# Kernel optimization log

Hardware: AMD Instinct MI355X
Metric: run time of the kernel (lower is better)

Reference implementation:

```python
import jax, jax.numpy as jnp
import numpy as np
from jax import lax

EPS = 1e-5      # BatchNorm1d default eps
SLOPE = 0.01    # LeakyReLU default negative_slope
DN = ('NCDHW', 'OIDHW', 'NCDHW')
PAD_31 = ((1, 1), (0, 0), (1, 1))   # kernel (3,1,3), padding (1,0,1)
PAD_13 = ((0, 0), (1, 1), (1, 1))   # kernel (1,3,3), padding (0,1,1)
PAD_P = ((1, 1), (1, 1), (1, 1))    # pool kernel 3, padding 1
STRIDE_P = (2, 2, 1)                # height_pooling=False -> stride (2,2,1)


def setup_inputs() -> dict:
    key = jax.random.key(0)
    ks = jax.random.split(key, 8)
    B, Cin, Cout = 1, 32, 64
    D1, D2, D3 = 160, 160, 32
    mask = jax.random.randint(ks[0], (B, 1, D1, D2, D3), 0, 2) > 0
    x = jax.random.normal(ks[1], (B, Cin, D1, D2, D3), dtype=jnp.float32)

    def w(k, cin, cout, kd, kh, kw):
        return jax.random.normal(k, (cout, cin, kd, kh, kw), dtype=jnp.float32) * 0.05

    inp = {
        'x': x, 'mask': mask,
        'W_A1': w(ks[2], Cin, Cout, 3, 1, 3),
        'W_A2': w(ks[3], Cout, Cout, 1, 3, 3),
        'W_B1': w(ks[4], Cin, Cout, 1, 3, 3),
        'W_B2': w(ks[5], Cout, Cout, 3, 1, 3),
        'W_pool': w(ks[6], Cout, Cout, 3, 3, 3),
    }
    for name in ('A1', 'A2', 'B1', 'B2'):
        inp['g_' + name] = jnp.ones((Cout,), jnp.float32)
        inp['b_' + name] = jnp.zeros((Cout,), jnp.float32)
    return inp


def _conv(h, W, pad, stride=(1, 1, 1)):
    return lax.conv_general_dilated(h, W, stride, pad, dimension_numbers=DN)


def _lrelu(h):
    return jnp.where(h >= 0, h, SLOPE * h)


def _masked_bn(h, m, n_active, gamma, beta):
    # BatchNorm1d over the [N_active, C] sparse feature tensor:
    # per-channel stats over active voxels only (biased variance, training mode).
    mean = jnp.sum(h * m, axis=(0, 2, 3, 4)) / n_active
    mu = mean[None, :, None, None, None]
    var = jnp.sum(((h - mu) ** 2) * m, axis=(0, 2, 3, 4)) / n_active
    inv = lax.rsqrt(var + EPS)[None, :, None, None, None]
    out = (h - mu) * inv * gamma[None, :, None, None, None] + beta[None, :, None, None, None]
    return out * m  # keep inactive sites exactly zero


def reference(x, mask, W_A1, W_A2, W_B1, W_B2, W_pool,
              g_A1, b_A1, g_A2, b_A2, g_B1, b_B1, g_B2, b_B2):
    m = mask.astype(x.dtype)                      # [B,1,D1,D2,D3] active-site indicator
    n_active = jnp.sum(m)
    xs = x * m                                    # sparse input: zero at inactive voxels

    def subm(h, W, pad):
        # submanifold conv: compute only at active output sites (same site set as input)
        return _conv(h, W, pad) * m

    # branch A: conv3x1 -> LeakyReLU -> BN -> conv1x3 -> LeakyReLU -> BN
    res_A = _masked_bn(_lrelu(subm(xs, W_A1, PAD_31)), m, n_active, g_A1, b_A1)
    res_A = _masked_bn(_lrelu(subm(res_A, W_A2, PAD_13)), m, n_active, g_A2, b_A2)

    # branch B: conv1x3 -> LeakyReLU -> BN -> conv3x1 -> LeakyReLU -> BN
    res_B = _masked_bn(_lrelu(subm(xs, W_B1, PAD_13)), m, n_active, g_B1, b_B1)
    res_B = _masked_bn(_lrelu(subm(res_B, W_B2, PAD_31)), m, n_active, g_B2, b_B2)

    res_B = res_B + res_A

    # strided SparseConv3d pool: output active where any input in 3x3x3 window is active
    ones_k = jnp.ones((1, 1, 3, 3, 3), x.dtype)
    out_mask = (_conv(m, ones_k, PAD_P, STRIDE_P) > 0).astype(x.dtype)
    down = _conv(res_B, W_pool, PAD_P, STRIDE_P) * out_mask
    return (down, res_B)
```

## Files before the change

kernel.cpp:

```cpp
#include <hip/hip_runtime.h>

static constexpr int ND1=160, ND2=160, ND3=32;
static constexpr int SP  = ND1*ND2*ND3;
static constexpr int CO  = 64;
static constexpr int OD1=80, OD2=80, OD3=32;
static constexpr int OSP = OD1*OD2*OD3;
static constexpr int NSC = 64;

typedef __attribute__((ext_vector_type(8))) short  short8;
typedef __attribute__((ext_vector_type(4))) float  f32x4;

__device__ __forceinline__ float b2f_lo(unsigned u){ return __uint_as_float(u<<16); }
__device__ __forceinline__ float b2f_hi(unsigned u){ return __uint_as_float(u & 0xffff0000u); }
__device__ __forceinline__ unsigned short f2b(float f){
    unsigned u = __float_as_uint(f);
    u += 0x7fffu + ((u>>16)&1u);
    return (unsigned short)(u>>16);
}
__device__ __forceinline__ unsigned cvtpk(float lo, float hi){
    unsigned r;
    asm("v_cvt_pk_bf16_f32 %0, %1, %2" : "=v"(r) : "v"(lo), "v"(hi));
    return r;
}
__device__ __forceinline__ float lrelu(float x){ return fmaxf(x, 0.01f*x); }

__global__ void k_detect(const unsigned char* __restrict__ mb, int* __restrict__ flag)
{
    __shared__ int lf;
    if (threadIdx.x == 0) lf = 0;
    __syncthreads();
    int f = 0;
    for (int i = blockIdx.x*256 + threadIdx.x; i < SP; i += gridDim.x*256) {
        unsigned char b = mb[i];
        if (b > 1) f |= 4;
        if (b != 0 && (i & 3)) f |= 1;
    }
    if (f) atomicOr(&lf, f);
    __syncthreads();
    if (threadIdx.x == 0 && lf) atomicOr(flag, lf);
}

__global__ void k_mask(const void* __restrict__ mraw, const int* __restrict__ flag,
                       float* __restrict__ m, float* __restrict__ nactN)
{
    int i = blockIdx.x*256 + threadIdx.x;
    int f = *flag;
    float v;
    if (f & 4)      v = (reinterpret_cast<const float*>(mraw)[i] != 0.f) ? 1.f : 0.f;
    else if (f & 1) v = (reinterpret_cast<const unsigned char*>(mraw)[i] != 0) ? 1.f : 0.f;
    else            v = (reinterpret_cast<const int*>(mraw)[i] != 0) ? 1.f : 0.f;
    m[i] = v;
    float s = v;
    #pragma unroll
    for (int off = 32; off > 0; off >>= 1) s += __shfl_xor(s, off);
    __shared__ float wsum[4];
    if ((threadIdx.x & 63) == 0) wsum[threadIdx.x >> 6] = s;
    __syncthreads();
    if (threadIdx.x == 0) atomicAdd(&nactN[blockIdx.x & (NSC-1)], wsum[0]+wsum[1]+wsum[2]+wsum[3]);
}

__global__ void k_finalize2(const float* __restrict__ SN0, const float* __restrict__ g0,
                            const float* __restrict__ b0, float* __restrict__ o0,
                            const float* __restrict__ SN1, const float* __restrict__ g1,
                            const float* __restrict__ b1, float* __restrict__ o1,
                            const float* __restrict__ nactN)
{
    const float* SN = blockIdx.x ? SN1 : SN0;
    const float* g  = blockIdx.x ? g1  : g0;
    const float* b  = blockIdx.x ? b1  : b0;
    float*       o  = blockIdx.x ? o1  : o0;
    int c = threadIdx.x;
    float s1 = 0.f, s2 = 0.f;
    #pragma unroll 4
    for (int k = 0; k < NSC; k++){
        s1 += SN[k*128 + c];
        s2 += SN[k*128 + 64 + c];
    }
    float nn = nactN[c];
    #pragma unroll
    for (int off = 32; off > 0; off >>= 1) nn += __shfl_xor(nn, off);
    float mean = s1 / nn;
    float var  = s2 / nn - mean*mean;
    float inv  = rsqrtf(var + 1e-5f);
    float sc   = inv * g[c];
    o[c]      = sc;
    o[64 + c] = b[c] - mean*sc;
}

__global__ void k_wprep_all(const float* __restrict__ WA1, const float* __restrict__ WA2,
                            const float* __restrict__ WB1, const float* __restrict__ WB2,
                            const float* __restrict__ WP,
                            unsigned short* __restrict__ tA1, unsigned short* __restrict__ tA2,
                            unsigned short* __restrict__ tB1, unsigned short* __restrict__ tB2,
                            unsigned short* __restrict__ tP)
{
    int i = blockIdx.x*256 + threadIdx.x;
    const float* W; unsigned short* Wt; int CIN, NT, base;
    if      (i < 18432)  { W=WA1; Wt=tA1; CIN=32; NT=9;  base=0; }
    else if (i < 55296)  { W=WA2; Wt=tA2; CIN=64; NT=9;  base=18432; }
    else if (i < 73728)  { W=WB1; Wt=tB1; CIN=32; NT=9;  base=55296; }
    else if (i < 110592) { W=WB2; Wt=tB2; CIN=64; NT=9;  base=73728; }
    else if (i < 221184) { W=WP;  Wt=tP;  CIN=64; NT=27; base=110592; }
    else return;
    int j = i - base;
    int ksub = j & 31;
    int t = j >> 5;
    int co = t & 63;
    int kc = t >> 6;
    int nch = CIN >> 5;
    int tap = kc / nch;
    int ci  = (kc - tap*nch)*32 + ksub;
    Wt[j] = f2b(W[((size_t)co*CIN + ci)*NT + tap]);
}

__global__ void k_prep_x(const float* __restrict__ x, const float* __restrict__ m,
                         unsigned short* __restrict__ xt, float* __restrict__ om)
{
    __shared__ float t[64][33];
    int sp0 = blockIdx.x*64;
    int tid = threadIdx.x;
    int c = tid>>6, s = tid&63;
    float mm = m[sp0+s];
    #pragma unroll
    for (int r=0;r<8;r++){
        int ci = c + r*4;
        t[s][ci] = x[(size_t)ci*SP + sp0 + s]*mm;
    }
    __syncthreads();
    int sp = tid>>2, c0 = (tid&3)*8;
    uint4 pk;
    pk.x = cvtpk(t[sp][c0+0], t[sp][c0+1]);
    pk.y = cvtpk(t[sp][c0+2], t[sp][c0+3]);
    pk.z = cvtpk(t[sp][c0+4], t[sp][c0+5]);
    pk.w = cvtpk(t[sp][c0+6], t[sp][c0+7]);
    *reinterpret_cast<uint4*>(xt + (size_t)(sp0+sp)*32 + c0) = pk;

    if (blockIdx.x < OSP/256){
        int i = blockIdx.x*256 + tid;
        int o3 = i & 31; int tt = i >> 5; int o2 = tt % OD2; int o1 = tt / OD2;
        float ssum = 0.f;
        for (int kd = 0; kd < 3; kd++) { int d1 = 2*o1 - 1 + kd; if ((unsigned)d1 >= ND1) continue;
          for (int kh = 0; kh < 3; kh++) { int d2 = 2*o2 - 1 + kh; if ((unsigned)d2 >= ND2) continue;
            for (int kw = 0; kw < 3; kw++) { int d3 = o3 - 1 + kw; if ((unsigned)d3 >= ND3) continue;
              ssum += m[(d1*ND2 + d2)*ND3 + d3];
            } } }
        om[i] = (ssum > 0.f) ? 1.f : 0.f;
    }
}

__global__ void k_resB(const unsigned short* __restrict__ hA, const unsigned short* __restrict__ hB,
                       const float* __restrict__ sA, const float* __restrict__ sB,
                       const float* __restrict__ m,
                       unsigned short* __restrict__ rbt, float* __restrict__ resf)
{
    __shared__ float t[64][65];
    __shared__ float ss[256];
    int tid = threadIdx.x;
    if (tid < 128){ ss[tid] = sA[tid]; ss[128+tid] = sB[tid]; }
    __syncthreads();
    int sp0 = blockIdx.x*64;
    int sp = tid>>2, c0 = (tid&3)*16;
    float mm = m[sp0+sp];
    const size_t base = (size_t)(sp0+sp)*64 + c0;
    uint4 a0 = *reinterpret_cast<const uint4*>(hA + base);
    uint4 a1 = *reinterpret_cast<const uint4*>(hA + base + 8);
    uint4 b0 = *reinterpret_cast<const uint4*>(hB + base);
    uint4 b1 = *reinterpret_cast<const uint4*>(hB + base + 8);
    unsigned pa4[8] = {a0.x,a0.y,a0.z,a0.w,a1.x,a1.y,a1.z,a1.w};
    unsigned pb4[8] = {b0.x,b0.y,b0.z,b0.w,b1.x,b1.y,b1.z,b1.w};
    float vv[16];
    #pragma unroll
    for (int q=0;q<8;q++){
        int ci = c0+q*2;
        float va0 = b2f_lo(pa4[q]), va1 = b2f_hi(pa4[q]);
        float vb0 = b2f_lo(pb4[q]), vb1 = b2f_hi(pb4[q]);
        float v0 = (va0*ss[ci]   + ss[64+ci]   + vb0*ss[128+ci]   + ss[192+ci])*mm;
        float v1 = (va1*ss[ci+1] + ss[64+ci+1] + vb1*ss[128+ci+1] + ss[192+ci+1])*mm;
        t[sp][ci] = v0; t[sp][ci+1] = v1;
        vv[q*2] = v0; vv[q*2+1] = v1;
    }
    uint4 p0, p1;
    p0.x = cvtpk(vv[0],vv[1]);   p0.y = cvtpk(vv[2],vv[3]);
    p0.z = cvtpk(vv[4],vv[5]);   p0.w = cvtpk(vv[6],vv[7]);
    p1.x = cvtpk(vv[8],vv[9]);   p1.y = cvtpk(vv[10],vv[11]);
    p1.z = cvtpk(vv[12],vv[13]); p1.w = cvtpk(vv[14],vv[15]);
    *reinterpret_cast<uint4*>(rbt + base)     = p0;
    *reinterpret_cast<uint4*>(rbt + base + 8) = p1;
    __syncthreads();
    int ci = tid>>2, s0 = (tid&3)*16;
    #pragma unroll
    for (int kq=0;kq<4;kq++){
        float4 ov;
        ov.x = t[s0+4*kq+0][ci]; ov.y = t[s0+4*kq+1][ci];
        ov.z = t[s0+4*kq+2][ci]; ov.w = t[s0+4*kq+3][ci];
        *reinterpret_cast<float4*>(resf + (size_t)ci*SP + sp0 + s0 + 4*kq) = ov;
    }
}

template<int CIN, bool HASAFF, int KA, int KB>
__launch_bounds__(256, 2)
__global__ void mconv_dual(const unsigned short* __restrict__ inA, const unsigned short* __restrict__ WtA,
                           const float* __restrict__ scshA, unsigned short* __restrict__ outA,
                           float* __restrict__ statsA,
                           const unsigned short* __restrict__ inB, const unsigned short* __restrict__ WtB,
                           const float* __restrict__ scshB, unsigned short* __restrict__ outB2,
                           float* __restrict__ statsB,
                           const float* __restrict__ mstage, const float* __restrict__ mout)
{
    constexpr int NCH  = CIN/32;
    constexpr int NR   = 10;
    constexpr int ROWB = 34*CIN*2;
    constexpr int SWZ  = (CIN==64) ? 7 : 3;
    constexpr int OBST = 144;
    constexpr int LDSZ = (NR*ROWB > 256*OBST) ? NR*ROWB : 256*OBST;
    __shared__ __align__(16) char lds[LDSZ];
    __shared__ float sst[128];

    const int tid = threadIdx.x;
    const int w = tid>>6, l = tid&63, g = l>>4, lj = l&15;

    const int bid  = blockIdx.x;
    const int hb   = (bid >= 3200) ? 1 : 0;
    const int b2   = bid - hb*3200;
    const int gi   = (b2&7)*400 + (b2>>3);
    const int kind = hb ? KB : KA;
    const unsigned short* in  = hb ? inB   : inA;
    const unsigned short* Wt  = hb ? WtB   : WtA;
    const float*        scsh  = hb ? scshB : scshA;
    unsigned short*     outb  = hb ? outB2 : outA;
    float*             statsN = hb ? statsB : statsA;

    int z  = gi % 160;
    int r0 = (gi / 160)*8;

    if (tid < 128) sst[tid] = 0.f;

    const int sd3 = tid>>3;
    const int k0  = (tid&7)*(CIN/8);

    float sc[8], sh[8];
    if (HASAFF){
        #pragma unroll
        for (int j=0;j<8;j++){ sc[j]=scsh[k0+j]; sh[j]=scsh[64+k0+j]; }
    }

    for (int i = tid; i < NR*2*(CIN/8); i += 256){
        int per = CIN/8;
        int rr = i / (2*per);
        int rem = i - rr*2*per;
        int slot = (rem >= per) ? 33 : 0;
        int kc16 = (rem >= per) ? (rem - per) : rem;
        int dst = rr*ROWB + slot*CIN*2 + kc16*16;
        dst ^= ((slot&SWZ)<<4);
        *reinterpret_cast<uint4*>(lds + dst) = make_uint4(0,0,0,0);
    }

    if (CIN==64){
        uint4 v[NR]; float mmr[NR];
        #pragma unroll
        for (int rr=0; rr<NR; rr++){
            int rw = r0 - 1 + rr;
            v[rr] = make_uint4(0,0,0,0); mmr[rr] = 0.f;
            if ((unsigned)rw < 160u){
                int vox = (kind==0) ? ((rw*ND2 + z)*ND3 + sd3)
                                    : ((z*ND2 + rw)*ND3 + sd3);
                v[rr] = *reinterpret_cast<const uint4*>(in + (size_t)vox*CIN + k0);
                if (HASAFF) mmr[rr] = mstage[vox];
            }
        }
        #pragma unroll
        for (int rr=0; rr<NR; rr++){
            uint4 vv = v[rr];
            if (HASAFF){
                float mm = mmr[rr];
                float q0 = (b2f_lo(vv.x)*sc[0]+sh[0])*mm;
                float q1 = (b2f_hi(vv.x)*sc[1]+sh[1])*mm;
                float q2 = (b2f_lo(vv.y)*sc[2]+sh[2])*mm;
                float q3 = (b2f_hi(vv.y)*sc[3]+sh[3])*mm;
                float q4 = (b2f_lo(vv.z)*sc[4]+sh[4])*mm;
                float q5 = (b2f_hi(vv.z)*sc[5]+sh[5])*mm;
                float q6 = (b2f_lo(vv.w)*sc[6]+sh[6])*mm;
                float q7 = (b2f_hi(vv.w)*sc[7]+sh[7])*mm;
                vv.x = cvtpk(q0,q1); vv.y = cvtpk(q2,q3);
                vv.z = cvtpk(q4,q5); vv.w = cvtpk(q6,q7);
            }
            int dst = (rr*ROWB + (((sd3+1)*CIN + k0)*2)) ^ (((sd3+1)&SWZ)<<4);
            *reinterpret_cast<uint4*>(lds + dst) = vv;
        }
    } else {
        uint2 v[NR];
        #pragma unroll
        for (int rr=0; rr<NR; rr++){
            int rw = r0 - 1 + rr;
            v[rr] = make_uint2(0,0);
            if ((unsigned)rw < 160u){
                int vox = (kind==0) ? ((rw*ND2 + z)*ND3 + sd3)
                                    : ((z*ND2 + rw)*ND3 + sd3);
                v[rr] = *reinterpret_cast<const uint2*>(in + (size_t)vox*CIN + k0);
            }
        }
        #pragma unroll
        for (int rr=0; rr<NR; rr++){
            int dst = (rr*ROWB + (((sd3+1)*CIN + k0)*2)) ^ (((sd3+1)&SWZ)<<4);
            *reinterpret_cast<uint2*>(lds + dst) = v[rr];
        }
    }

    int tb[4];
    #pragma unroll
    for (int t=0;t<4;t++){
        int rowb = w*2 + (t>>1);
        int o3   = (t&1)*16 + lj;
        tb[t] = rowb*ROWB + ((o3*CIN + g*8)*2);
    }

    __syncthreads();

    f32x4 acc[4][4];
    #pragma unroll
    for (int c=0;c<4;c++)
        #pragma unroll
        for (int t=0;t<4;t++)
            #pragma unroll
            for (int q=0;q<4;q++) acc[c][t][q] = 0.f;

    const unsigned short* wb = Wt + lj*32 + g*8;

    #pragma unroll 1
    for (int ch=0; ch<NCH; ch++){
        short8 pa[9][4];
        #pragma unroll
        for (int tap=0; tap<9; tap++){
            const int kc = tap*NCH + ch;
            #pragma unroll
            for (int ct=0; ct<4; ct++)
                pa[tap][ct] = *reinterpret_cast<const short8*>(wb + (size_t)kc*2048 + ct*512);
        }
        int f[3];
        #pragma unroll
        for (int kw=0;kw<3;kw++){
            int x   = (lj+kw)&SWZ;
            int fld = (CIN==64) ? (g + 4*ch) : g;
            f[kw] = kw*CIN*2 + ((CIN==64) ? ch*64 : 0) + (((fld ^ x) - fld) << 4);
        }
        #pragma unroll
        for (int tap=0; tap<9; tap++){
            const int kd = tap/3, kw = tap - kd*3;
            #pragma unroll
            for (int t=0;t<4;t++){
                short8 bv = *reinterpret_cast<const short8*>(lds + kd*ROWB + tb[t] + f[kw]);
                #pragma unroll
                for (int ct=0; ct<4; ct++)
                    acc[ct][t] = __builtin_amdgcn_mfma_f32_16x16x32_bf16(pa[tap][ct], bv, acc[ct][t], 0,0,0);
            }
        }
    }

    __syncthreads();

    float mmv[4];
    #pragma unroll
    for (int t=0;t<4;t++){
        int rowb = w*2 + (t>>1);
        int o3   = (t&1)*16 + lj;
        int o2r  = r0 + rowb;
        int ovox = (kind==0) ? ((o2r*ND2 + z)*ND3 + o3)
                             : ((z*ND2 + o2r)*ND3 + o3);
        mmv[t] = mout[ovox];
    }
    #pragma unroll
    for (int ct=0;ct<4;ct++){
        float s1[4] = {0.f,0.f,0.f,0.f};
        float s2[4] = {0.f,0.f,0.f,0.f};
        #pragma unroll
        for (int t=0;t<4;t++){
            int rowb = w*2 + (t>>1);
            int o3   = (t&1)*16 + lj;
            int vloc = rowb*32 + o3;
            float v[4];
            #pragma unroll
            for (int r=0;r<4;r++){
                float xv = lrelu(acc[ct][t][r]*mmv[t]);
                v[r] = xv; s1[r] += xv; s2[r] += xv*xv;
            }
            *reinterpret_cast<uint2*>(lds + vloc*OBST + (ct*16 + g*4)*2) =
                make_uint2(cvtpk(v[0],v[1]), cvtpk(v[2],v[3]));
        }
        #pragma unroll
        for (int r=0;r<4;r++){
            float a = s1[r], b = s2[r];
            a += __shfl_xor(a,1); b += __shfl_xor(b,1);
            a += __shfl_xor(a,2); b += __shfl_xor(b,2);
            a += __shfl_xor(a,4); b += __shfl_xor(b,4);
            a += __shfl_xor(a,8); b += __shfl_xor(b,8);
            if (lj == 0){
                atomicAdd(&sst[ct*16 + g*4 + r], a);
                atomicAdd(&sst[64 + ct*16 + g*4 + r], b);
            }
        }
    }
    __syncthreads();
    #pragma unroll
    for (int i=0;i<8;i++){
        int idx = i*256 + tid;
        int vloc = idx >> 3;
        int q    = idx & 7;
        int row  = vloc >> 5;
        int o3g  = vloc & 31;
        int gvox = (kind==0) ? (((r0+row)*ND2 + z)*ND3 + o3g)
                             : ((z*ND2 + (r0+row))*ND3 + o3g);
        uint4 v = *reinterpret_cast<uint4*>(lds + vloc*OBST + q*16);
        *reinterpret_cast<uint4*>(outb + (size_t)gvox*64 + q*8) = v;
    }
    if (tid < 128){
        float* sg = statsN + (size_t)(blockIdx.x & (NSC-1))*128;
        atomicAdd(&sg[tid], sst[tid]);
    }
}

__launch_bounds__(256, 2)
__global__ void mpool5(const unsigned short* __restrict__ in,
                       const unsigned short* __restrict__ Wt,
                       const float* __restrict__ mout,
                       float* __restrict__ outf)
{
    constexpr int SLOTB = 80;
    constexpr int ROWB  = 34*SLOTB;
    extern __shared__ __align__(16) char lds[];

    const int tid = threadIdx.x;
    const int w = tid>>6, l = tid&63, g = l>>4, lj = l&15;
    const int h = w&1, rg = w>>1;

    int gi = (blockIdx.x & 7)*(gridDim.x>>3) + (blockIdx.x>>3);
    int z  = gi % OD1;
    int r0 = (gi / OD1)*4;

    const int sd3 = tid>>3;
    const int kq  = tid&7;

    for (int i = tid; i < 27*2*4; i += 256){
        int row = i >> 3, rem = i & 7;
        int slot = (rem >= 4) ? 33 : 0;
        int c16 = rem & 3;
        *reinterpret_cast<uint4*>(lds + row*ROWB + slot*SLOTB + c16*16) = make_uint4(0,0,0,0);
    }

    int ovx[4];
    float om[4];
    #pragma unroll
    for (int t=0;t<4;t++){
        int row = rg*2 + (t>>1);
        int o3  = (t&1)*16 + lj;
        ovx[t] = (z*OD2 + (r0 + row))*OD3 + o3;
        om[t]  = mout[ovx[t]];
    }

    f32x4 acc[2][4];
    #pragma unroll
    for (int c=0;c<2;c++)
        #pragma unroll
        for (int t=0;t<4;t++)
            #pragma unroll
            for (int q=0;q<4;q++) acc[c][t][q] = 0.f;

    const unsigned short* wbase = Wt + (size_t)(h*32)*32 + lj*32 + g*8;

    #pragma unroll 1
    for (int ph=0; ph<2; ph++){
        uint2 v[27];
        #pragma unroll
        for (int i=0;i<27;i++){
            const int kd = i/9, rr = i - (i/9)*9;
            int d1 = 2*z - 1 + kd;
            int d2 = 2*r0 - 1 + rr;
            v[i] = make_uint2(0,0);
            if ((unsigned)d1 < (unsigned)ND1 && (unsigned)d2 < (unsigned)ND2){
                int vox = (d1*ND2 + d2)*ND3 + sd3;
                v[i] = *reinterpret_cast<const uint2*>(in + (size_t)vox*64 + ph*32 + kq*4);
            }
        }
        __syncthreads();
        #pragma unroll
        for (int i=0;i<27;i++){
            *reinterpret_cast<uint2*>(lds + i*ROWB + (sd3+1)*SLOTB + kq*8) = v[i];
        }
        __syncthreads();

        #pragma unroll
        for (int kd=0; kd<3; kd++){
            short8 pa[9][2];
            #pragma unroll
            for (int tap=0; tap<9; tap++){
                const int kc = (kd*9 + tap)*2 + ph;
                pa[tap][0] = *reinterpret_cast<const short8*>(wbase + (size_t)kc*2048);
                pa[tap][1] = *reinterpret_cast<const short8*>(wbase + (size_t)kc*2048 + 512);
            }
            #pragma unroll
            for (int tap=0; tap<9; tap++){
                const int kh = tap/3, kw = tap - (tap/3)*3;
                #pragma unroll
                for (int t=0;t<4;t++){
                    const int rr = 2*(rg*2 + (t>>1)) + kh;
                    const int slot = (t&1)*16 + lj + kw;
                    const char* bp = lds + (kd*9 + rr)*ROWB + slot*SLOTB + g*16;
                    short8 bv = *reinterpret_cast<const short8*>(bp);
                    acc[0][t] = __builtin_amdgcn_mfma_f32_16x16x32_bf16(pa[tap][0], bv, acc[0][t], 0,0,0);
                    acc[1][t] = __builtin_amdgcn_mfma_f32_16x16x32_bf16(pa[tap][1], bv, acc[1][t], 0,0,0);
                }
            }
        }
    }

    __syncthreads();
    float* olds = (float*)lds;
    #pragma unroll
    for (int c=0;c<2;c++){
        const int ct = h*2 + c;
        #pragma unroll
        for (int t=0;t<4;t++){
            int row = rg*2 + (t>>1);
            int o3  = (t&1)*16 + lj;
            #pragma unroll
            for (int r=0;r<4;r++){
                int co = ct*16 + g*4 + r;
                olds[co*128 + row*32 + o3] = acc[c][t][r]*om[t];
            }
        }
    }
    __syncthreads();
    const size_t obase = (size_t)(z*OD2 + r0)*OD3;
    #pragma unroll
    for (int i=0;i<8;i++){
        int idx = i*256 + tid;
        int co  = idx >> 5;
        int q   = idx & 31;
        uint4 v = *reinterpret_cast<uint4*>(reinterpret_cast<char*>(olds) + co*512 + q*16);
        *reinterpret_cast<uint4*>(outf + (size_t)co*OSP + obase + q*4) = v;
    }
}

extern "C" void kernel_launch(void* const* d_in, const int* in_sizes, int n_in,
                              void* d_out, int out_size, void* d_ws, size_t ws_size,
                              hipStream_t stream)
{
    const float* x      = (const float*)d_in[0];
    const void*  mraw   = d_in[1];
    const float* W_A1   = (const float*)d_in[2];
    const float* W_A2   = (const float*)d_in[3];
    const float* W_B1   = (const float*)d_in[4];
    const float* W_B2   = (const float*)d_in[5];
    const float* W_pool = (const float*)d_in[6];
    const float* g_A1 = (const float*)d_in[7],  *b_A1 = (const float*)d_in[8];
    const float* g_A2 = (const float*)d_in[9],  *b_A2 = (const float*)d_in[10];
    const float* g_B1 = (const float*)d_in[11], *b_B1 = (const float*)d_in[12];
    const float* g_B2 = (const float*)d_in[13], *b_B2 = (const float*)d_in[14];

    char* p = (char*)d_ws;
    float* m     = (float*)p; p += (size_t)SP*4;
    float* omask = (float*)p; p += (size_t)OSP*4;
    float* statsN= (float*)p; p += 4*NSC*128*4;
    float* scsh  = (float*)p; p += 4*128*4;
    float* nactN = (float*)p; p += NSC*4;
    int*   flag  = (int*)p;   p += 4;
    p += 252;
    unsigned short* WtA1 = (unsigned short*)p; p += 288*64*2;
    unsigned short* WtA2 = (unsigned short*)p; p += 576*64*2;
    unsigned short* WtB1 = (unsigned short*)p; p += 288*64*2;
    unsigned short* WtB2 = (unsigned short*)p; p += 576*64*2;
    unsigned short* WtP  = (unsigned short*)p; p += 1728*64*2;
    unsigned short* X = (unsigned short*)p; p += (size_t)SP*32*2;
    unsigned short* P = (unsigned short*)p; p += (size_t)SP*64*2;
    unsigned short* Q = (unsigned short*)p; p += (size_t)SP*64*2;
    unsigned short* R = (unsigned short*)p; p += (size_t)SP*64*2;
    unsigned short* S = (unsigned short*)p; p += (size_t)SP*64*2;

    float* down = (float*)d_out;
    float* resf = down + (size_t)CO*OSP;

    const int shmP = 27*34*80;
    hipFuncSetAttribute((const void*)&mpool5, hipFuncAttributeMaxDynamicSharedMemorySize, shmP);

    hipMemsetAsync(statsN, 0, (4*NSC*128 + 4*128 + NSC)*4 + 4, stream);
    k_detect<<<256, 256, 0, stream>>>((const unsigned char*)mraw, flag);
    k_mask<<<SP/256, 256, 0, stream>>>(mraw, flag, m, nactN);
    k_wprep_all<<<864, 256, 0, stream>>>(W_A1, W_A2, W_B1, W_B2, W_pool,
                                         WtA1, WtA2, WtB1, WtB2, WtP);
    k_prep_x<<<SP/64, 256, 0, stream>>>(x, m, X, omask);

    float* SA1 = statsN + 0*NSC*128;
    float* SA2 = statsN + 1*NSC*128;
    float* SB1 = statsN + 2*NSC*128;
    float* SB2 = statsN + 3*NSC*128;

    mconv_dual<32,false,0,1><<<6400, 256, 0, stream>>>(
        X, WtA1, nullptr, P, SA1,
        X, WtB1, nullptr, Q, SB1, nullptr, m);
    k_finalize2<<<2, 64, 0, stream>>>(SA1, g_A1, b_A1, scsh + 0,
                                      SB1, g_B1, b_B1, scsh + 256, nactN);
    mconv_dual<64,true,1,0><<<6400, 256, 0, stream>>>(
        P, WtA2, scsh + 0,   R, SA2,
        Q, WtB2, scsh + 256, S, SB2, m, m);
    k_finalize2<<<2, 64, 0, stream>>>(SA2, g_A2, b_A2, scsh + 128,
                                      SB2, g_B2, b_B2, scsh + 384, nactN);
    k_resB<<<SP/64, 256, 0, stream>>>(R, S, scsh + 128, scsh + 384, m, Q, resf);
    mpool5<<<1600, 256, shmP, stream>>>(Q, WtP, omask, down);
}
```

Measured before the change: 636.9 us.

## Switch dual submanifold conv to 32x32x16 MFMA tiles and raise occupancy

New measurement: 715.7 us. 12.4% more time.

```diff
diff --git a/kernel.cpp b/kernel.cpp
--- a/kernel.cpp
+++ b/kernel.cpp
@@ -7,8 +7,9 @@
 static constexpr int OSP = OD1*OD2*OD3;
 static constexpr int NSC = 64;
 
-typedef __attribute__((ext_vector_type(8))) short  short8;
-typedef __attribute__((ext_vector_type(4))) float  f32x4;
+typedef __attribute__((ext_vector_type(8)))  short  short8;
+typedef __attribute__((ext_vector_type(4)))  float  f32x4;
+typedef __attribute__((ext_vector_type(16))) float  f32x16;
 
 __device__ __forceinline__ float b2f_lo(unsigned u){ return __uint_as_float(u<<16); }
 __device__ __forceinline__ float b2f_hi(unsigned u){ return __uint_as_float(u & 0xffff0000u); }
@@ -95,22 +96,32 @@
                             unsigned short* __restrict__ tP)
 {
     int i = blockIdx.x*256 + threadIdx.x;
-    const float* W; unsigned short* Wt; int CIN, NT, base;
-    if      (i < 18432)  { W=WA1; Wt=tA1; CIN=32; NT=9;  base=0; }
-    else if (i < 55296)  { W=WA2; Wt=tA2; CIN=64; NT=9;  base=18432; }
-    else if (i < 73728)  { W=WB1; Wt=tB1; CIN=32; NT=9;  base=55296; }
-    else if (i < 110592) { W=WB2; Wt=tB2; CIN=64; NT=9;  base=73728; }
-    else if (i < 221184) { W=WP;  Wt=tP;  CIN=64; NT=27; base=110592; }
-    else return;
-    int j = i - base;
-    int ksub = j & 31;
-    int t = j >> 5;
-    int co = t & 63;
-    int kc = t >> 6;
-    int nch = CIN >> 5;
-    int tap = kc / nch;
-    int ci  = (kc - tap*nch)*32 + ksub;
-    Wt[j] = f2b(W[((size_t)co*CIN + ci)*NT + tap]);
+    if (i < 110592){
+        const float* W; unsigned short* Wt; int CIN, base;
+        if      (i < 18432)  { W=WA1; Wt=tA1; CIN=32; base=0; }
+        else if (i < 55296)  { W=WA2; Wt=tA2; CIN=64; base=18432; }
+        else if (i < 73728)  { W=WB1; Wt=tB1; CIN=32; base=55296; }
+        else                 { W=WB2; Wt=tB2; CIN=64; base=73728; }
+        int j = i - base;
+        int k   = j & 15;
+        int t   = j >> 4;
+        int co  = t & 63;
+        int kci = t >> 6;
+        int nk16 = CIN >> 4;
+        int tap = kci / nk16;
+        int k16 = kci - tap*nk16;
+        int ci  = k16*16 + k;
+        Wt[j] = f2b(W[((size_t)co*CIN + ci)*9 + tap]);
+    } else if (i < 221184){
+        int j = i - 110592;
+        int ksub = j & 31;
+        int t = j >> 5;
+        int co = t & 63;
+        int kc = t >> 6;
+        int tap = kc / 2;
+        int ci  = (kc - tap*2)*32 + ksub;
+        tP[j] = f2b(WP[((size_t)co*64 + ci)*27 + tap]);
+    }
 }
 
 __global__ void k_prep_x(const float* __restrict__ x, const float* __restrict__ m,
@@ -198,7 +209,7 @@
 }
 
 template<int CIN, bool HASAFF, int KA, int KB>
-__launch_bounds__(256, 2)
+__launch_bounds__(256, 3)
 __global__ void mconv_dual(const unsigned short* __restrict__ inA, const unsigned short* __restrict__ WtA,
                            const float* __restrict__ scshA, unsigned short* __restrict__ outA,
                            float* __restrict__ statsA,
@@ -207,7 +218,7 @@
                            float* __restrict__ statsB,
                            const float* __restrict__ mstage, const float* __restrict__ mout)
 {
-    constexpr int NCH  = CIN/32;
+    constexpr int NK16 = CIN/16;
     constexpr int NR   = 10;
     constexpr int ROWB = 34*CIN*2;
     constexpr int SWZ  = (CIN==64) ? 7 : 3;
@@ -217,7 +228,8 @@
     __shared__ float sst[128];
 
     const int tid = threadIdx.x;
-    const int w = tid>>6, l = tid&63, g = l>>4, lj = l&15;
+    const int w = tid>>6, l = tid&63;
+    const int cl = l & 31, hf = l >> 5;
 
     const int bid  = blockIdx.x;
     const int hb   = (bid >= 3200) ? 1 : 0;
@@ -306,96 +318,94 @@
         }
     }
 
-    int tb[4];
-    #pragma unroll
-    for (int t=0;t<4;t++){
-        int rowb = w*2 + (t>>1);
-        int o3   = (t&1)*16 + lj;
-        tb[t] = rowb*ROWB + ((o3*CIN + g*8)*2);
-    }
-
-    __syncthreads();
-
-    f32x4 acc[4][4];
-    #pragma unroll
-    for (int c=0;c<4;c++)
-        #pragma unroll
-        for (int t=0;t<4;t++)
-            #pragma unroll
-            for (int q=0;q<4;q++) acc[c][t][q] = 0.f;
-
-    const unsigned short* wb = Wt + lj*32 + g*8;
+    int tb0[2];
+    #pragma unroll
+    for (int tr=0;tr<2;tr++)
+        tb0[tr] = (2*w+tr)*ROWB + cl*CIN*2 + hf*16;
+
+    __syncthreads();
+
+    f32x16 acc[2][2];
+    #pragma unroll
+    for (int ct=0;ct<2;ct++)
+        #pragma unroll
+        for (int tr=0;tr<2;tr++)
+            #pragma unroll
+            for (int q=0;q<16;q++) acc[ct][tr][q] = 0.f;
+
+    const unsigned short* wb = Wt + cl*16 + hf*8;
 
     #pragma unroll 1
-    for (int ch=0; ch<NCH; ch++){
-        short8 pa[9][4];
+    for (int k16=0; k16<NK16; k16++){
+        short8 pa[9][2];
         #pragma unroll
         for (int tap=0; tap<9; tap++){
-            const int kc = tap*NCH + ch;
-            #pragma unroll
-            for (int ct=0; ct<4; ct++)
-                pa[tap][ct] = *reinterpret_cast<const short8*>(wb + (size_t)kc*2048 + ct*512);
+            const int kci = tap*NK16 + k16;
+            pa[tap][0] = *reinterpret_cast<const short8*>(wb + (size_t)kci*1024);
+            pa[tap][1] = *reinterpret_cast<const short8*>(wb + (size_t)kci*1024 + 512);
         }
         int f[3];
         #pragma unroll
         for (int kw=0;kw<3;kw++){
-            int x   = (lj+kw)&SWZ;
-            int fld = (CIN==64) ? (g + 4*ch) : g;
-            f[kw] = kw*CIN*2 + ((CIN==64) ? ch*64 : 0) + (((fld ^ x) - fld) << 4);
+            int s7  = ((l & SWZ) + kw) & SWZ;
+            int fld = (k16*2 + hf) & SWZ;
+            f[kw] = kw*CIN*2 + k16*32 + (((fld ^ s7) - fld) << 4);
         }
         #pragma unroll
         for (int tap=0; tap<9; tap++){
             const int kd = tap/3, kw = tap - kd*3;
             #pragma unroll
-            for (int t=0;t<4;t++){
-                short8 bv = *reinterpret_cast<const short8*>(lds + kd*ROWB + tb[t] + f[kw]);
-                #pragma unroll
-                for (int ct=0; ct<4; ct++)
-                    acc[ct][t] = __builtin_amdgcn_mfma_f32_16x16x32_bf16(pa[tap][ct], bv, acc[ct][t], 0,0,0);
-            }
-        }
-    }
-
-    __syncthreads();
-
-    float mmv[4];
-    #pragma unroll
-    for (int t=0;t<4;t++){
-        int rowb = w*2 + (t>>1);
-        int o3   = (t&1)*16 + lj;
-        int o2r  = r0 + rowb;
-        int ovox = (kind==0) ? ((o2r*ND2 + z)*ND3 + o3)
-                             : ((z*ND2 + o2r)*ND3 + o3);
-        mmv[t] = mout[ovox];
-    }
-    #pragma unroll
-    for (int ct=0;ct<4;ct++){
-        float s1[4] = {0.f,0.f,0.f,0.f};
-        float s2[4] = {0.f,0.f,0.f,0.f};
-        #pragma unroll
-        for (int t=0;t<4;t++){
-            int rowb = w*2 + (t>>1);
-            int o3   = (t&1)*16 + lj;
-            int vloc = rowb*32 + o3;
-            float v[4];
-            #pragma unroll
-            for (int r=0;r<4;r++){
-                float xv = lrelu(acc[ct][t][r]*mmv[t]);
-                v[r] = xv; s1[r] += xv; s2[r] += xv*xv;
-            }
-            *reinterpret_cast<uint2*>(lds + vloc*OBST + (ct*16 + g*4)*2) =
-                make_uint2(cvtpk(v[0],v[1]), cvtpk(v[2],v[3]));
-        }
-        #pragma unroll
-        for (int r=0;r<4;r++){
+            for (int tr=0;tr<2;tr++){
+                short8 bv = *reinterpret_cast<const short8*>(lds + kd*ROWB + tb0[tr] + f[kw]);
+                acc[0][tr] = __builtin_amdgcn_mfma_f32_32x32x16_bf16(pa[tap][0], bv, acc[0][tr], 0,0,0);
+                acc[1][tr] = __builtin_amdgcn_mfma_f32_32x32x16_bf16(pa[tap][1], bv, acc[1][tr], 0,0,0);
+            }
+        }
+    }
+
+    __syncthreads();
+
+    float mmv[2];
+    #pragma unroll
+    for (int tr=0;tr<2;tr++){
+        int o2r  = r0 + 2*w + tr;
+        int ovox = (kind==0) ? ((o2r*ND2 + z)*ND3 + cl)
+                             : ((z*ND2 + o2r)*ND3 + cl);
+        mmv[tr] = mout[ovox];
+    }
+    #pragma unroll
+    for (int ct=0;ct<2;ct++){
+        float s1[16], s2[16];
+        #pragma unroll
+        for (int r=0;r<16;r++){ s1[r]=0.f; s2[r]=0.f; }
+        #pragma unroll
+        for (int tr=0;tr<2;tr++){
+            int vloc = (2*w+tr)*32 + cl;
+            float xv[16];
+            #pragma unroll
+            for (int r=0;r<16;r++){
+                float v = lrelu(acc[ct][tr][r]*mmv[tr]);
+                xv[r] = v; s1[r] += v; s2[r] += v*v;
+            }
+            #pragma unroll
+            for (int rg4=0;rg4<4;rg4++){
+                int cob = ct*32 + 8*rg4 + 4*hf;
+                *reinterpret_cast<uint2*>(lds + vloc*OBST + cob*2) =
+                    make_uint2(cvtpk(xv[rg4*4+0],xv[rg4*4+1]), cvtpk(xv[rg4*4+2],xv[rg4*4+3]));
+            }
+        }
+        #pragma unroll
+        for (int r=0;r<16;r++){
             float a = s1[r], b = s2[r];
-            a += __shfl_xor(a,1); b += __shfl_xor(b,1);
-            a += __shfl_xor(a,2); b += __shfl_xor(b,2);
-            a += __shfl_xor(a,4); b += __shfl_xor(b,4);
-            a += __shfl_xor(a,8); b += __shfl_xor(b,8);
-            if (lj == 0){
-                atomicAdd(&sst[ct*16 + g*4 + r], a);
-                atomicAdd(&sst[64 + ct*16 + g*4 + r], b);
+            a += __shfl_xor(a,1);  b += __shfl_xor(b,1);
+            a += __shfl_xor(a,2);  b += __shfl_xor(b,2);
+            a += __shfl_xor(a,4);  b += __shfl_xor(b,4);
+            a += __shfl_xor(a,8);  b += __shfl_xor(b,8);
+            a += __shfl_xor(a,16); b += __shfl_xor(b,16);
+            if (cl == 0){
+                int co = ct*32 + (r&3) + 8*(r>>2) + 4*hf;
+                atomicAdd(&sst[co], a);
+                atomicAdd(&sst[64 + co], b);
             }
         }
     }
```
